# Performance work log

Hardware: AMD Instinct MI355X
Metric: run time of the kernel (lower is better)

The kernel has to match this reference:

```python
import jax, jax.numpy as jnp
import numpy as np

Q_DIM = 768
KV_DIM = 1024
NUM_HEADS = 12
HEAD_DIM = Q_DIM // NUM_HEADS  # 64


def setup_inputs() -> dict:
    key = jax.random.key(0)
    ks = jax.random.split(key, 10)
    B, N_q, N_kv = 16, 64, 4096
    s_q = 1.0 / np.sqrt(Q_DIM)
    s_kv = 1.0 / np.sqrt(KV_DIM)
    return {
        "query": jax.random.normal(ks[0], (B, N_q, Q_DIM), dtype=jnp.float32),
        "kv": jax.random.normal(ks[1], (B, N_kv, KV_DIM), dtype=jnp.float32),
        "Wq": jax.random.normal(ks[2], (Q_DIM, Q_DIM), dtype=jnp.float32) * s_q,
        "bq": jnp.zeros((Q_DIM,), dtype=jnp.float32),
        "Wk": jax.random.normal(ks[3], (KV_DIM, Q_DIM), dtype=jnp.float32) * s_kv,
        "bk": jnp.zeros((Q_DIM,), dtype=jnp.float32),
        "Wv": jax.random.normal(ks[4], (KV_DIM, Q_DIM), dtype=jnp.float32) * s_kv,
        "bv": jnp.zeros((Q_DIM,), dtype=jnp.float32),
        "Wo": jax.random.normal(ks[5], (Q_DIM, Q_DIM), dtype=jnp.float32) * s_q,
        "bo": jnp.zeros((Q_DIM,), dtype=jnp.float32),
    }


def reference(query, kv, Wq, bq, Wk, bk, Wv, bv, Wo, bo):
    B, N_q, C = query.shape
    N_kv = kv.shape[1]
    H, D = NUM_HEADS, HEAD_DIM
    scale = D ** -0.5
    # projections -> (B, H, N, D)
    q = (query @ Wq + bq).reshape(B, N_q, H, D).transpose(0, 2, 1, 3)
    k = (kv @ Wk + bk).reshape(B, N_kv, H, D).transpose(0, 2, 1, 3)
    v = (kv @ Wv + bv).reshape(B, N_kv, H, D).transpose(0, 2, 1, 3)
    # scores (B, H, N_q, N_kv) -- explicitly materialized as in the original
    attn = jnp.einsum("bhqd,bhkd->bhqk", q, k) * scale
    attn = jax.nn.softmax(attn, axis=-1)
    x = jnp.einsum("bhqk,bhkd->bhqd", attn, v)
    x = x.transpose(0, 2, 1, 3).reshape(B, N_q, C)
    return x @ Wo + bo
```

## Files before the change

### kernel.cpp

```cpp
#include <hip/hip_runtime.h>
#include <hip/hip_bf16.h>

typedef unsigned short u16;
typedef unsigned int u32;
typedef short v8s __attribute__((ext_vector_type(8)));
typedef float v4f __attribute__((ext_vector_type(4)));

#define NB 16
#define NQ 64
#define NKV 4096
#define QD 768
#define KD 1024
#define NH 12
#define HD 64

__device__ __forceinline__ u16 f2bf(float f) {
  union { float f; u32 u; } c; c.f = f;
  u32 u = c.u;
  u += 0x7FFFu + ((u >> 16) & 1u);
  return (u16)(u >> 16);
}
__device__ __forceinline__ u32 pack2(float a, float b) {
  return (u32)f2bf(a) | ((u32)f2bf(b) << 16);
}

__device__ __forceinline__ void async16(const void* g, void* l) {
  __builtin_amdgcn_global_load_lds(
      (const __attribute__((address_space(1))) void*)g,
      (__attribute__((address_space(3))) void*)l, 16, 0, 0);
}

__global__ __launch_bounds__(256) void prep_wT_dual(
    const float* __restrict__ W0, const float* __restrict__ W1,
    u16* __restrict__ T0, u16* __restrict__ T1, int K, int N) {
  __shared__ float tile[32][33];
  const float* W = blockIdx.z ? W1 : W0;
  u16* WT = blockIdx.z ? T1 : T0;
  const int n0 = blockIdx.x * 32, k0 = blockIdx.y * 32;
  const int tr = threadIdx.x >> 5, tc = threadIdx.x & 31;
#pragma unroll
  for (int r = tr; r < 32; r += 8) tile[r][tc] = W[(size_t)(k0 + r) * N + n0 + tc];
  __syncthreads();
#pragma unroll
  for (int r = tr; r < 32; r += 8) WT[(size_t)(n0 + r) * K + k0 + tc] = f2bf(tile[tc][r]);
}

__global__ __launch_bounds__(256) void conv8(const float* __restrict__ s,
                                             u16* __restrict__ d, int n8) {
  int i = blockIdx.x * 256 + threadIdx.x;
  if (i >= n8) return;
  const float4* sp = (const float4*)s + (size_t)i * 2;
  float4 a = sp[0], b = sp[1];
  uint4 o;
  o.x = pack2(a.x, a.y); o.y = pack2(a.z, a.w);
  o.z = pack2(b.x, b.y); o.w = pack2(b.z, b.w);
  ((uint4*)d)[i] = o;
}

__global__ void concat_bias(const float* __restrict__ a, const float* __restrict__ b,
                            float* __restrict__ o) {
  int i = blockIdx.x * 256 + threadIdx.x;
  if (i < 768) o[i] = a[i];
  else if (i < 1536) o[i] = b[i - 768];
}

template<bool OUT_BF16, bool KV_SPLIT>
__global__ __launch_bounds__(256) void gemm_a(
    const u16* __restrict__ A, const u16* __restrict__ BT,
    const float* __restrict__ bias, void* __restrict__ Cp, u16* __restrict__ Vtp,
    int M, int N, int K)
{
  __shared__ __align__(16) u16 As[128][32];
  __shared__ __align__(16) u16 Bs[128][32];
  const int bn0 = blockIdx.x * 128, bm0 = blockIdx.y * 128;
  const int t = threadIdx.x, lane = t & 63, wv = t >> 6;
  const int wm = (wv & 1) * 64, wn = (wv >> 1) * 64;
  const int lm = lane & 15, quad = lane >> 4;
  const int srow = lane >> 2;
  const int sc = (((lane & 3) ^ ((srow >> 1) & 3)) * 8);

  const int r0 = wv * 32, r1 = wv * 32 + 16;
  const u16* aP0 = A  + (size_t)(bm0 + r0 + srow) * K + sc;
  const u16* aP1 = A  + (size_t)(bm0 + r1 + srow) * K + sc;
  const u16* bP0 = BT + (size_t)(bn0 + r0 + srow) * K + sc;
  const u16* bP1 = BT + (size_t)(bn0 + r1 + srow) * K + sc;

  const int swz = (lm >> 1) & 3;

  v4f acc[4][4];
  v4f zero = {0.f, 0.f, 0.f, 0.f};
#pragma unroll
  for (int i = 0; i < 4; ++i)
#pragma unroll
    for (int j = 0; j < 4; ++j) acc[i][j] = zero;

  for (int k0 = 0; k0 < K; k0 += 32) {
    async16(aP0, &As[r0][0]);
    async16(aP1, &As[r1][0]);
    async16(bP0, &Bs[r0][0]);
    async16(bP1, &Bs[r1][0]);
    aP0 += 32; aP1 += 32; bP0 += 32; bP1 += 32;
    __builtin_amdgcn_s_waitcnt(0);
    __syncthreads();
    v8s a[4], b[4];
#pragma unroll
    for (int mt = 0; mt < 4; ++mt)
      a[mt] = *(const v8s*)&As[wm + mt * 16 + lm][(quad ^ swz) * 8];
#pragma unroll
    for (int nt = 0; nt < 4; ++nt)
      b[nt] = *(const v8s*)&Bs[wn + nt * 16 + lm][(quad ^ swz) * 8];
#pragma unroll
    for (int mt = 0; mt < 4; ++mt)
#pragma unroll
      for (int nt = 0; nt < 4; ++nt)
        acc[mt][nt] = __builtin_amdgcn_mfma_f32_16x16x32_bf16(a[mt], b[nt], acc[mt][nt], 0, 0, 0);
    __syncthreads();
  }

  if constexpr (KV_SPLIT) {
    if (bn0 < 768) {
      u16* kp_ = (u16*)Cp;
#pragma unroll
      for (int mt = 0; mt < 4; ++mt)
#pragma unroll
        for (int nt = 0; nt < 4; ++nt) {
          int col = bn0 + wn + nt * 16 + lm;
          float bs = bias[col];
#pragma unroll
          for (int r = 0; r < 4; ++r) {
            int grow = bm0 + wm + mt * 16 + quad * 4 + r;
            kp_[(size_t)grow * 768 + col] = f2bf(acc[mt][nt][r] + bs);
          }
        }
    } else {
#pragma unroll
      for (int mt = 0; mt < 4; ++mt)
#pragma unroll
        for (int nt = 0; nt < 4; ++nt) {
          int col = bn0 + wn + nt * 16 + lm;
          int cv = col - 768;
          float bs = bias[col];
          int grow0 = bm0 + wm + mt * 16 + quad * 4;
          int b_ = grow0 >> 12, kvr = grow0 & 4095;
          uint2 o;
          o.x = pack2(acc[mt][nt][0] + bs, acc[mt][nt][1] + bs);
          o.y = pack2(acc[mt][nt][2] + bs, acc[mt][nt][3] + bs);
          *(uint2*)&Vtp[((size_t)(b_ * 768 + cv)) * 4096 + kvr] = o;
        }
    }
  } else {
#pragma unroll
    for (int mt = 0; mt < 4; ++mt)
#pragma unroll
      for (int nt = 0; nt < 4; ++nt)
#pragma unroll
        for (int r = 0; r < 4; ++r) {
          int row = bm0 + wm + mt * 16 + quad * 4 + r;
          int col = bn0 + wn + nt * 16 + lm;
          float v = acc[mt][nt][r] + bias[col];
          if constexpr (OUT_BF16) ((u16*)Cp)[(size_t)row * N + col] = f2bf(v);
          else                    ((float*)Cp)[(size_t)row * N + col] = v;
        }
  }
}

#define KVK 1024
#define KVKT 16
#define SLOT 32768

__global__ __launch_bounds__(512, 2) void gemm_kv256(
    const u16* __restrict__ A, const u16* __restrict__ BT,
    const float* __restrict__ bias,
    u16* __restrict__ kp_, u16* __restrict__ vT_)
{
  __shared__ __align__(16) u16 As[2][256][64];
  __shared__ __align__(16) u16 Bs[2][256][64];

  const int bid = blockIdx.x;
  const int swzb = (bid & 7) * 192 + (bid >> 3);
  const int tn = swzb % 6, tm = swzb / 6;
  const int bn0 = tn * 256, bm0 = tm * 256;

  const int tid = threadIdx.x;
  const int lane = tid & 63, wv = tid >> 6;
  const int lm = lane & 15, quad = lane >> 4;
  const int wrow = wv >> 2, wcol = wv & 3;

  const int srow = tid >> 3;
  const int schunk = (tid & 7) ^ (srow & 7);
  const u16* aS = A  + (size_t)(bm0 + srow) * KVK + schunk * 8;
  const u16* bS = BT + (size_t)(bn0 + srow) * KVK + schunk * 8;
  char* const aD = (char*)&As[0][0][0] + wv * 1024;
  char* const bD = (char*)&Bs[0][0][0] + wv * 1024;

  const int c0 = (quad ^ (lm & 7)) * 16;
  const int c1 = ((quad + 4) ^ (lm & 7)) * 16;
  const char* const aR = (const char*)&As[0][0][0] + (wrow * 128 + lm) * 128;
  const char* const bR = (const char*)&Bs[0][0][0] + (wcol * 64 + lm) * 128;

  v4f acc[8][4];
  v4f zero = {0.f, 0.f, 0.f, 0.f};
#pragma unroll
  for (int i = 0; i < 8; ++i)
#pragma unroll
    for (int j = 0; j < 4; ++j) acc[i][j] = zero;

#pragma unroll
  for (int r = 0; r < 4; ++r) {
    async16(aS + (size_t)r * (64 * KVK), aD + r * 8192);
    async16(bS + (size_t)r * (64 * KVK), bD + r * 8192);
  }
  aS += 64; bS += 64;
  __syncthreads();

  int soff = 0;
#pragma unroll 1
  for (int t = 0; t < KVKT; ++t) {
    const int noff = soff ^ SLOT;
    if (t + 1 < KVKT) {
#pragma unroll
      for (int r = 0; r < 4; ++r) {
        async16(aS + (size_t)r * (64 * KVK), aD + noff + r * 8192);
        async16(bS + (size_t)r * (64 * KVK), bD + noff + r * 8192);
      }
      aS += 64; bS += 64;
    }
    v8s bf[4][2];
#pragma unroll
    for (int nt = 0; nt < 4; ++nt) {
      const char* bp = bR + soff + nt * 2048;
      bf[nt][0] = *(const v8s*)(bp + c0);
      bf[nt][1] = *(const v8s*)(bp + c1);
    }
#pragma unroll
    for (int p = 0; p < 4; ++p) {
      v8s af[2][2];
#pragma unroll
      for (int i = 0; i < 2; ++i) {
        const char* ap = aR + soff + (p * 2 + i) * 2048;
        af[i][0] = *(const v8s*)(ap + c0);
        af[i][1] = *(const v8s*)(ap + c1);
      }
      __builtin_amdgcn_s_barrier();
      asm volatile("s_waitcnt lgkmcnt(0)" ::: "memory");
      __builtin_amdgcn_sched_barrier(0);
      __builtin_amdgcn_s_setprio(1);
#pragma unroll
      for (int i = 0; i < 2; ++i)
#pragma unroll
        for (int nt = 0; nt < 4; ++nt) {
          acc[p * 2 + i][nt] = __builtin_amdgcn_mfma_f32_16x16x32_bf16(
              af[i][0], bf[nt][0], acc[p * 2 + i][nt], 0, 0, 0);
          acc[p * 2 + i][nt] = __builtin_amdgcn_mfma_f32_16x16x32_bf16(
              af[i][1], bf[nt][1], acc[p * 2 + i][nt], 0, 0, 0);
        }
      __builtin_amdgcn_s_setprio(0);
      __builtin_amdgcn_s_barrier();
    }
    __syncthreads();
    soff = noff;
  }

  if (bn0 < 768) {
#pragma unroll
    for (int mt = 0; mt < 8; ++mt)
#pragma unroll
      for (int nt = 0; nt < 4; ++nt) {
        const int col = bn0 + wcol * 64 + nt * 16 + lm;
        const float bs = bias[col];
        const int grow0 = bm0 + wrow * 128 + mt * 16 + quad * 4;
#pragma unroll
        for (int r = 0; r < 4; ++r)
          kp_[(size_t)(grow0 + r) * 768 + col] = f2bf(acc[mt][nt][r] + bs);
      }
  } else {
#pragma unroll
    for (int mt = 0; mt < 8; ++mt)
#pragma unroll
      for (int nt = 0; nt < 4; ++nt) {
        const int col = bn0 + wcol * 64 + nt * 16 + lm;
        const int cv = col - 768;
        const float bs = bias[col];
        const int grow0 = bm0 + wrow * 128 + mt * 16 + quad * 4;
        const int b_ = grow0 >> 12, kvr = grow0 & 4095;
        uint2 o;
        o.x = pack2(acc[mt][nt][0] + bs, acc[mt][nt][1] + bs);
        o.y = pack2(acc[mt][nt][2] + bs, acc[mt][nt][3] + bs);
        *(uint2*)&vT_[((size_t)(b_ * 768 + cv)) * 4096 + kvr] = o;
      }
  }
}

__global__ __launch_bounds__(256) void attn_k(
    const u16* __restrict__ qp,
    const u16* __restrict__ kp,
    const u16* __restrict__ vT,
    u16* __restrict__ xo)
{
  __shared__ __align__(16) u16 Ps[4][16][40];
  __shared__ float Mw[4][16], Lw[4][16];
  __shared__ float Os[4][16][64];
  const int lane = threadIdx.x & 63, w = threadIdx.x >> 6;
  const int lm = lane & 15, quad = lane >> 4;
  const int blk = blockIdx.x, slab = blk & 3, bh = blk >> 2;
  const int b = bh / NH, h = bh - b * NH;
  const int qr0 = b * NQ + slab * 16;

  const u16* qptr = qp + (size_t)(qr0 + lm) * QD + h * HD + quad * 8;
  v8s aq0 = *(const v8s*)qptr;
  v8s aq1 = *(const v8s*)(qptr + 32);

  const u16* kb = kp + (size_t)b * NKV * QD + h * HD;
  const u16* vb = vT + (size_t)(b * QD + h * HD) * NKV;

  float mst[4], lst[4];
  v4f O[4];
  v4f zero = {0.f, 0.f, 0.f, 0.f};
#pragma unroll
  for (int r = 0; r < 4; ++r) { mst[r] = -INFINITY; lst[r] = 0.f; }
#pragma unroll
  for (int d = 0; d < 4; ++d) O[d] = zero;

  const float scale = 0.125f;

  v8s kf[2][4], vf[2][4];
  auto loadchunk = [&](int j0, int bi) {
    const u16* k0p = kb + (size_t)(j0 + lm) * QD + quad * 8;
    const u16* k1p = kb + (size_t)(j0 + 16 + lm) * QD + quad * 8;
    kf[bi][0] = *(const v8s*)k0p;
    kf[bi][1] = *(const v8s*)(k0p + 32);
    kf[bi][2] = *(const v8s*)k1p;
    kf[bi][3] = *(const v8s*)(k1p + 32);
#pragma unroll
    for (int d = 0; d < 4; ++d)
      vf[bi][d] = *(const v8s*)&vb[(size_t)(d * 16 + lm) * NKV + j0 + quad * 8];
  };
  auto compute = [&](int bi) {
    v4f S0 = zero, S1 = zero;
    S0 = __builtin_amdgcn_mfma_f32_16x16x32_bf16(aq0, kf[bi][0], S0, 0, 0, 0);
    S0 = __builtin_amdgcn_mfma_f32_16x16x32_bf16(aq1, kf[bi][1], S0, 0, 0, 0);
    S1 = __builtin_amdgcn_mfma_f32_16x16x32_bf16(aq0, kf[bi][2], S1, 0, 0, 0);
    S1 = __builtin_amdgcn_mfma_f32_16x16x32_bf16(aq1, kf[bi][3], S1, 0, 0, 0);

    float p0[4], p1[4], rmax[4];
#pragma unroll
    for (int r = 0; r < 4; ++r) {
      p0[r] = S0[r] * scale; p1[r] = S1[r] * scale;
      rmax[r] = fmaxf(p0[r], p1[r]);
    }
#pragma unroll
    for (int off = 1; off <= 8; off <<= 1)
#pragma unroll
      for (int r = 0; r < 4; ++r) rmax[r] = fmaxf(rmax[r], __shfl_xor(rmax[r], off, 64));

    float alpha[4], rsum[4];
#pragma unroll
    for (int r = 0; r < 4; ++r) {
      float mn = fmaxf(mst[r], rmax[r]);
      alpha[r] = __expf(mst[r] - mn);
      p0[r] = __expf(p0[r] - mn);
      p1[r] = __expf(p1[r] - mn);
      mst[r] = mn;
      rsum[r] = p0[r] + p1[r];
    }
#pragma unroll
    for (int off = 1; off <= 8; off <<= 1)
#pragma unroll
      for (int r = 0; r < 4; ++r) rsum[r] += __shfl_xor(rsum[r], off, 64);
#pragma unroll
    for (int r = 0; r < 4; ++r) {
      lst[r] = lst[r] * alpha[r] + rsum[r];
      Ps[w][quad * 4 + r][lm] = f2bf(p0[r]);
      Ps[w][quad * 4 + r][16 + lm] = f2bf(p1[r]);
    }
#pragma unroll
    for (int d = 0; d < 4; ++d)
#pragma unroll
      for (int r = 0; r < 4; ++r) O[d][r] *= alpha[r];
    v8s aP = *(const v8s*)&Ps[w][lm][quad * 8];
#pragma unroll
    for (int d = 0; d < 4; ++d)
      O[d] = __builtin_amdgcn_mfma_f32_16x16x32_bf16(aP, vf[bi][d], O[d], 0, 0, 0);
  };

  const int base = w * 1024;
  loadchunk(base, 0);
  for (int j0 = base; j0 < base + 1024; j0 += 64) {
    loadchunk(j0 + 32, 1);
    compute(0);
    if (j0 + 64 < base + 1024) loadchunk(j0 + 64, 0);
    compute(1);
  }

  if (lm == 0) {
#pragma unroll
    for (int r = 0; r < 4; ++r) {
      Mw[w][quad * 4 + r] = mst[r];
      Lw[w][quad * 4 + r] = lst[r];
    }
  }
  __syncthreads();
#pragma unroll
  for (int r = 0; r < 4; ++r) {
    int row = quad * 4 + r;
    float M = fmaxf(fmaxf(Mw[0][row], Mw[1][row]), fmaxf(Mw[2][row], Mw[3][row]));
    float sc = __expf(mst[r] - M);
#pragma unroll
    for (int d = 0; d < 4; ++d) Os[w][row][d * 16 + lm] = O[d][r] * sc;
  }
  __syncthreads();
#pragma unroll
  for (int i = 0; i < 4; ++i) {
    int row = w * 4 + i;
    float M = fmaxf(fmaxf(Mw[0][row], Mw[1][row]), fmaxf(Mw[2][row], Mw[3][row]));
    float L = Lw[0][row] * __expf(Mw[0][row] - M) + Lw[1][row] * __expf(Mw[1][row] - M)
            + Lw[2][row] * __expf(Mw[2][row] - M) + Lw[3][row] * __expf(Mw[3][row] - M);
    float o = Os[0][row][lane] + Os[1][row][lane] + Os[2][row][lane] + Os[3][row][lane];
    xo[(size_t)(qr0 + row) * QD + h * HD + lane] = f2bf(o / L);
  }
}

extern "C" void kernel_launch(void* const* d_in, const int* in_sizes, int n_in,
                              void* d_out, int out_size, void* d_ws, size_t ws_size,
                              hipStream_t stream) {
  const float* query = (const float*)d_in[0];
  const float* kv    = (const float*)d_in[1];
  const float* Wq    = (const float*)d_in[2];
  const float* bq    = (const float*)d_in[3];
  const float* Wk    = (const float*)d_in[4];
  const float* bk    = (const float*)d_in[5];
  const float* Wv    = (const float*)d_in[6];
  const float* bv    = (const float*)d_in[7];
  const float* Wo    = (const float*)d_in[8];
  const float* bo    = (const float*)d_in[9];
  float* out = (float*)d_out;
  char* ws = (char*)d_ws;

  u16*   WkvT = (u16*)(ws);
  float* bkv  = (float*)(ws + 3145728);
  u16*   WqT  = (u16*)(ws + 3151872);
  u16*   WoT  = (u16*)(ws + 4331520);
  u16*   qbf  = (u16*)(ws + 5511168);
  u16*   qp   = (u16*)(ws + 7084032);
  u16*   xov  = (u16*)(ws + 8656896);
  u16*   kp   = (u16*)(ws + 10229760);
  u16*   vT   = (u16*)(ws + 110893056);
  u16*   kvbf = (u16*)(ws + 211556352);

  prep_wT_dual<<<dim3(24, 32, 2), 256, 0, stream>>>(Wk, Wv, WkvT, WkvT + 768 * 1024, KD, QD);
  prep_wT_dual<<<dim3(24, 24, 2), 256, 0, stream>>>(Wq, Wo, WqT, WoT, QD, QD);
  concat_bias<<<6, 256, 0, stream>>>(bk, bv, bkv);
  conv8<<<32768, 256, 0, stream>>>(kv, kvbf, NB * NKV * KD / 8);
  gemm_kv256<<<1536, 512, 0, stream>>>(kvbf, WkvT, bkv, kp, vT);
  conv8<<<384, 256, 0, stream>>>(query, qbf, NB * NQ * QD / 8);
  gemm_a<true, false><<<dim3(6, 8), 256, 0, stream>>>(qbf, WqT, bq, qp, nullptr,
                                                      1024, QD, QD);
  attn_k<<<NB * NH * 4, 256, 0, stream>>>(qp, kp, vT, xov);
  gemm_a<false, false><<<dim3(6, 8), 256, 0, stream>>>(xov, WoT, bo, out, nullptr,
                                                       1024, QD, QD);
}
```

Measured before the change: 897.6 us.

## Deepen KV projection GEMM pipeline to four-stage K=32 ring buffer

```diff
diff --git a/kernel.cpp b/kernel.cpp
--- a/kernel.cpp
+++ b/kernel.cpp
@@ -165,16 +165,16 @@
 }
 
 #define KVK 1024
-#define KVKT 16
-#define SLOT 32768
+#define KT32 32
+#define SLOTB 16384
 
 __global__ __launch_bounds__(512, 2) void gemm_kv256(
     const u16* __restrict__ A, const u16* __restrict__ BT,
     const float* __restrict__ bias,
     u16* __restrict__ kp_, u16* __restrict__ vT_)
 {
-  __shared__ __align__(16) u16 As[2][256][64];
-  __shared__ __align__(16) u16 Bs[2][256][64];
+  __shared__ __align__(16) u16 As[4][256][32];
+  __shared__ __align__(16) u16 Bs[4][256][32];
 
   const int bid = blockIdx.x;
   const int swzb = (bid & 7) * 192 + (bid >> 3);
@@ -186,17 +186,16 @@
   const int lm = lane & 15, quad = lane >> 4;
   const int wrow = wv >> 2, wcol = wv & 3;
 
-  const int srow = tid >> 3;
-  const int schunk = (tid & 7) ^ (srow & 7);
-  const u16* aS = A  + (size_t)(bm0 + srow) * KVK + schunk * 8;
-  const u16* bS = BT + (size_t)(bn0 + srow) * KVK + schunk * 8;
+  const int srow = tid >> 2;
+  const int schunk = (tid & 3) ^ ((srow >> 1) & 3);
+  const u16* const aS = A  + (size_t)(bm0 + srow) * KVK + schunk * 8;
+  const u16* const bS = BT + (size_t)(bn0 + srow) * KVK + schunk * 8;
   char* const aD = (char*)&As[0][0][0] + wv * 1024;
   char* const bD = (char*)&Bs[0][0][0] + wv * 1024;
 
-  const int c0 = (quad ^ (lm & 7)) * 16;
-  const int c1 = ((quad + 4) ^ (lm & 7)) * 16;
-  const char* const aR = (const char*)&As[0][0][0] + (wrow * 128 + lm) * 128;
-  const char* const bR = (const char*)&Bs[0][0][0] + (wcol * 64 + lm) * 128;
+  const int cA = (quad ^ ((lm >> 1) & 3)) * 16;
+  const char* const aR = (const char*)&As[0][0][0] + (wrow * 128 + lm) * 64;
+  const char* const bR = (const char*)&Bs[0][0][0] + (wcol * 64 + lm) * 64;
 
   v4f acc[8][4];
   v4f zero = {0.f, 0.f, 0.f, 0.f};
@@ -205,60 +204,59 @@
 #pragma unroll
     for (int j = 0; j < 4; ++j) acc[i][j] = zero;
 
-#pragma unroll
-  for (int r = 0; r < 4; ++r) {
-    async16(aS + (size_t)r * (64 * KVK), aD + r * 8192);
-    async16(bS + (size_t)r * (64 * KVK), bD + r * 8192);
-  }
-  aS += 64; bS += 64;
-  __syncthreads();
-
-  int soff = 0;
+  auto issueA = [&](int t) {
+    const u16* s = aS + (size_t)t * 32;
+    char* d = aD + (t & 3) * SLOTB;
+    async16(s, d);
+    async16(s + (size_t)128 * KVK, d + 8192);
+  };
+  auto issueB = [&](int t) {
+    const u16* s = bS + (size_t)t * 32;
+    char* d = bD + (t & 3) * SLOTB;
+    async16(s, d);
+    async16(s + (size_t)128 * KVK, d + 8192);
+  };
+
+#pragma unroll
+  for (int t = 0; t < 3; ++t) { issueA(t); issueB(t); }
+
 #pragma unroll 1
-  for (int t = 0; t < KVKT; ++t) {
-    const int noff = soff ^ SLOT;
-    if (t + 1 < KVKT) {
-#pragma unroll
-      for (int r = 0; r < 4; ++r) {
-        async16(aS + (size_t)r * (64 * KVK), aD + noff + r * 8192);
-        async16(bS + (size_t)r * (64 * KVK), bD + noff + r * 8192);
-      }
-      aS += 64; bS += 64;
-    }
-    v8s bf[4][2];
-#pragma unroll
-    for (int nt = 0; nt < 4; ++nt) {
-      const char* bp = bR + soff + nt * 2048;
-      bf[nt][0] = *(const v8s*)(bp + c0);
-      bf[nt][1] = *(const v8s*)(bp + c1);
-    }
-#pragma unroll
-    for (int p = 0; p < 4; ++p) {
-      v8s af[2][2];
-#pragma unroll
-      for (int i = 0; i < 2; ++i) {
-        const char* ap = aR + soff + (p * 2 + i) * 2048;
-        af[i][0] = *(const v8s*)(ap + c0);
-        af[i][1] = *(const v8s*)(ap + c1);
-      }
-      __builtin_amdgcn_s_barrier();
-      asm volatile("s_waitcnt lgkmcnt(0)" ::: "memory");
-      __builtin_amdgcn_sched_barrier(0);
-      __builtin_amdgcn_s_setprio(1);
-#pragma unroll
-      for (int i = 0; i < 2; ++i)
-#pragma unroll
-        for (int nt = 0; nt < 4; ++nt) {
-          acc[p * 2 + i][nt] = __builtin_amdgcn_mfma_f32_16x16x32_bf16(
-              af[i][0], bf[nt][0], acc[p * 2 + i][nt], 0, 0, 0);
-          acc[p * 2 + i][nt] = __builtin_amdgcn_mfma_f32_16x16x32_bf16(
-              af[i][1], bf[nt][1], acc[p * 2 + i][nt], 0, 0, 0);
-        }
-      __builtin_amdgcn_s_setprio(0);
-      __builtin_amdgcn_s_barrier();
-    }
-    __syncthreads();
-    soff = noff;
+  for (int t = 0; t < KT32; ++t) {
+    const int so = (t & 3) * SLOTB;
+    if (t < KT32 - 2)       asm volatile("s_waitcnt vmcnt(8)" ::: "memory");
+    else if (t == KT32 - 2) asm volatile("s_waitcnt vmcnt(4)" ::: "memory");
+    else                    asm volatile("s_waitcnt vmcnt(0)" ::: "memory");
+    __builtin_amdgcn_sched_barrier(0);
+    __builtin_amdgcn_s_barrier();
+
+    if (t + 3 < KT32) issueA(t + 3);
+    v8s bf[4], af[4];
+#pragma unroll
+    for (int nt = 0; nt < 4; ++nt) bf[nt] = *(const v8s*)(bR + so + nt * 1024 + cA);
+#pragma unroll
+    for (int i = 0; i < 4; ++i)    af[i] = *(const v8s*)(aR + so + i * 1024 + cA);
+    asm volatile("s_waitcnt lgkmcnt(0)" ::: "memory");
+    __builtin_amdgcn_sched_barrier(0);
+    __builtin_amdgcn_s_setprio(1);
+#pragma unroll
+    for (int i = 0; i < 4; ++i)
+#pragma unroll
+      for (int nt = 0; nt < 4; ++nt)
+        acc[i][nt] = __builtin_amdgcn_mfma_f32_16x16x32_bf16(af[i], bf[nt], acc[i][nt], 0, 0, 0);
+    __builtin_amdgcn_s_setprio(0);
+    __builtin_amdgcn_s_barrier();
+    if (t + 3 < KT32) issueB(t + 3);
+#pragma unroll
+    for (int i = 0; i < 4; ++i)    af[i] = *(const v8s*)(aR + so + (4 + i) * 1024 + cA);
+    asm volatile("s_waitcnt lgkmcnt(0)" ::: "memory");
+    __builtin_amdgcn_sched_barrier(0);
+    __builtin_amdgcn_s_setprio(1);
+#pragma unroll
+    for (int i = 0; i < 4; ++i)
+#pragma unroll
+      for (int nt = 0; nt < 4; ++nt)
+        acc[4 + i][nt] = __builtin_amdgcn_mfma_f32_16x16x32_bf16(af[i], bf[nt], acc[4 + i][nt], 0, 0, 0);
+    __builtin_amdgcn_s_setprio(0);
   }
 
   if (bn0 < 768) {
```

New measurement: 885.3 us. Within noise of the previous version (-1.4%).
